# Performance work log

Measured on AMD Instinct MI355X. Metric: run time of the kernel, lower is better.

Reference implementation:

```python
import jax, jax.numpy as jnp
import numpy as np
from jax import lax

DN = ("NCDHW", "OIDHW", "NCDHW")


def bn(x, g, b, eps=1e-5):
    # torch BatchNorm3d training-mode forward: biased batch stats over (N, *, spatial)
    axes = (0,) + tuple(range(2, x.ndim))
    m = x.mean(axes, keepdims=True)
    v = x.var(axes, keepdims=True)
    shp = (1, -1) + (1,) * (x.ndim - 2)
    return (x - m) * lax.rsqrt(v + eps) * g.reshape(shp) + b.reshape(shp)


def conv_bn_relu(x, w, g, b, stride=(1, 1, 1), pad=(1, 0, 0)):
    y = lax.conv_general_dilated(x, w, stride, [(p, p) for p in pad], dimension_numbers=DN)
    return jax.nn.relu(bn(y, g, b))


def pw_bn_relu(x, w, g, b):  # 1x1x1 conv (no bias) + BN + ReLU on (B,C,T,H,W)
    y = jnp.einsum('oi,bithw->bothw', w, x)
    return jax.nn.relu(bn(y, g, b))


def pam_enc(x, pe_w, pe_g, pe_b):
    b, c, t, h, w = x.shape
    xm = x.mean(axis=2)  # all adaptive pools have T_out = 1
    feats = []
    for i, s in enumerate((1, 2, 3, 6)):  # H,W chosen divisible by 1,2,3,6 -> exact block means
        p = xm.reshape(b, c, s, h // s, s, w // s).mean(axis=(3, 5))  # (B,C,s,s)
        f = jnp.einsum('oi,bihw->bohw', pe_w[i], p)
        f = jax.nn.relu(bn(f, pe_g[i], pe_b[i]))
        feats.append(f.reshape(b, c, s * s))
    return jnp.concatenate(feats, axis=2)  # (B, C, 1+4+9+36=50)


def pam_dec(x, y, wq, bq, wk, bk, wv, bv, scale):
    # x: (B,C,T,H,W), y: (B,K,C)
    b, c, t, h, w = x.shape
    n = t * h * w
    q = jnp.einsum('oi,bithw->bothw', wq, x) + bq.reshape(1, -1, 1, 1, 1)
    q = q.reshape(b, c // 4, n).transpose(0, 2, 1)            # (B,N,C/4)
    k = y @ wk.T + bk                                         # (B,K,C/4)
    attn = jax.nn.softmax(jnp.einsum('bnd,bkd->bnk', q, k), axis=-1)
    v = y @ wv.T + bv                                         # (B,K,C)
    out = jnp.einsum('bkc,bnk->bcn', v, attn).reshape(b, c, t, h, w)
    return scale * out + x


def cam_dec(x, y, scale):
    b, c, t, h, w = x.shape
    xf = x.reshape(b, c, -1)
    yf = y.reshape(b, y.shape[1], -1)
    energy = jnp.einsum('bcn,bkn->bck', xf, yf)               # (B,C,K)
    attn = jax.nn.softmax(energy.max(-1, keepdims=True) - energy, axis=-1)
    out = jnp.einsum('bck,bkn->bcn', attn, yf).reshape(b, c, t, h, w)
    return x + scale * out


def tam_dec(x, y, scale):
    xp = x.transpose(0, 2, 1, 3, 4)  # (B,T,C,H,W)
    yp = y.transpose(0, 2, 1, 3, 4)
    b, t, c, h, w = xp.shape
    xf = xp.reshape(b, t, -1)
    yf = yp.reshape(b, t, -1)
    energy = jnp.einsum('bim,bjm->bij', xf, yf)               # (B,T,T)
    attn = jax.nn.softmax(energy.max(-1, keepdims=True) - energy, axis=-1)
    out = jnp.einsum('bij,bjm->bim', attn, yf).reshape(b, t, c, h, w)
    return (xp + scale * out).transpose(0, 2, 1, 3, 4)


def caf(x1, x2, w_conv1, g_conv1, b_conv1, w_conv2, g_conv2, b_conv2, w_tam, g_tam, b_tam, w_cat, g_cat, b_cat, pe_w, pe_g, pe_b, pd_wq, pd_bq, pd_wk, pd_bk, pd_wv, pd_bv, pd_scale, ce_w, ce_g, ce_b, cd_scale, te_w, te_g, te_b, td_scale):
    c1 = lambda z: conv_bn_relu(z, w_conv1, g_conv1, b_conv1)
    c2 = lambda z: conv_bn_relu(z, w_conv2, g_conv2, b_conv2)
    x1i = c1(x1)  # conv1(x1) is used by both PAM and CAM branches (identical in torch)
    x2i = c1(x2)
    # PAM branches
    x1_pa = c2(pam_dec(x1i, pam_enc(x1i, pe_w, pe_g, pe_b).transpose(0, 2, 1), pd_wq, pd_bq, pd_wk, pd_bk, pd_wv, pd_bv, pd_scale))
    x2_pa = c2(pam_dec(x2i, pam_enc(x2i, pe_w, pe_g, pe_b).transpose(0, 2, 1), pd_wq, pd_bq, pd_wk, pd_bk, pd_wv, pd_bv, pd_scale))
    # CAM branches
    x1_ca = c2(cam_dec(x1i, pw_bn_relu(x1i, ce_w, ce_g, ce_b), cd_scale))
    x2_ca = c2(cam_dec(x2i, pw_bn_relu(x2i, ce_w, ce_g, ce_b), cd_scale))
    # TAM branch over temporal concat (2T frames)
    xt1 = c1(jnp.concatenate([x1, x2], axis=2))
    xt2 = pw_bn_relu(xt1, te_w, te_g, te_b)
    x_ta = conv_bn_relu(tam_dec(xt1, xt2, td_scale), w_tam, g_tam, b_tam, stride=(2, 1, 1))
    out1 = conv_bn_relu(jnp.concatenate([x1_pa, x2_ca, x_ta], axis=1), w_cat, g_cat, b_cat)
    out2 = conv_bn_relu(jnp.concatenate([x2_pa, x1_ca, x_ta], axis=1), w_cat, g_cat, b_cat)
    return out1, out2


def setup_inputs() -> dict:
    key = jax.random.key(0)
    B, C, T, H, W = 4, 256, 16, 36, 36
    IC = C // 4
    ks = iter(jax.random.split(key, 24))
    rn = lambda shape, s=0.05: jax.random.normal(next(ks), shape, jnp.float32) * s
    ones = lambda n: jnp.ones((n,), jnp.float32)
    zeros = lambda n: jnp.zeros((n,), jnp.float32)
    return {
        "x1": rn((B, C, T, H, W), 1.0),
        "x2": rn((B, C, T, H, W), 1.0),
        "w_conv1": rn((IC, C, 3, 1, 1)), "g_conv1": ones(IC), "b_conv1": zeros(IC),
        "w_conv2": rn((IC, IC, 3, 1, 1)), "g_conv2": ones(IC), "b_conv2": zeros(IC),
        "w_tam": rn((IC, IC, 3, 1, 1)), "g_tam": ones(IC), "b_tam": zeros(IC),
        "w_cat": rn((C, 3 * IC, 3, 1, 1)), "g_cat": ones(C), "b_cat": zeros(C),
        "pe_w": rn((4, IC, IC)), "pe_g": jnp.ones((4, IC), jnp.float32), "pe_b": jnp.zeros((4, IC), jnp.float32),
        "pd_wq": rn((IC // 4, IC)), "pd_bq": zeros(IC // 4),
        "pd_wk": rn((IC // 4, IC)), "pd_bk": zeros(IC // 4),
        "pd_wv": rn((IC, IC)), "pd_bv": zeros(IC),
        "pd_scale": jnp.full((1,), 0.1, jnp.float32),
        "ce_w": rn((IC // 16, IC)), "ce_g": ones(IC // 16), "ce_b": zeros(IC // 16),
        "cd_scale": jnp.full((1,), 0.1, jnp.float32),
        "te_w": rn((IC, IC)), "te_g": ones(IC), "te_b": zeros(IC),
        "td_scale": jnp.full((1,), 0.1, jnp.float32),
    }


def reference(x1, x2, w_conv1, g_conv1, b_conv1, w_conv2, g_conv2, b_conv2, w_tam, g_tam, b_tam, w_cat, g_cat, b_cat, pe_w, pe_g, pe_b, pd_wq, pd_bq, pd_wk, pd_bk, pd_wv, pd_bv, pd_scale, ce_w, ce_g, ce_b, cd_scale, te_w, te_g, te_b, td_scale):
    return caf(x1, x2, w_conv1, g_conv1, b_conv1, w_conv2, g_conv2, b_conv2, w_tam, g_tam, b_tam, w_cat, g_cat, b_cat, pe_w, pe_g, pe_b, pd_wq, pd_bq, pd_wk, pd_bk, pd_wv, pd_bv, pd_scale, ce_w, ce_g, ce_b, cd_scale, te_w, te_g, te_b, td_scale)
```

## Files before the change

### kernel.cpp

```cpp
#include <hip/hip_runtime.h>

#define HW 1296
#define Tt 16
#define T2 32
#define Nn 20736
#define N2 41472
#define TAPAD 72

typedef short bf16x8 __attribute__((ext_vector_type(8)));
typedef float f32x4 __attribute__((ext_vector_type(4)));

__device__ inline unsigned short f2b(float f){
  union { float f; unsigned u; } v; v.f = f;
  unsigned r = v.u + 0x7FFF + ((v.u >> 16) & 1);
  return (unsigned short)(r >> 16);
}
__device__ inline float b2f(unsigned short u){
  union { unsigned u; float f; } v; v.u = ((unsigned)u) << 16; return v.f;
}
__device__ inline float b2f_lo(unsigned u){
  union { unsigned u; float f; } v; v.u = u << 16; return v.f;
}
__device__ inline float b2f_hi(unsigned u){
  union { unsigned u; float f; } v; v.u = u & 0xffff0000u; return v.f;
}

__device__ __forceinline__ void pack_pairs(const float* a, unsigned* vals){
  #pragma unroll
  for (int i = 0; i < 32; ++i)
    vals[i] = (unsigned)f2b(a[2*i]) | ((unsigned)f2b(a[2*i+1]) << 16);
}

__device__ __forceinline__ void staged_write(unsigned* lds, int tid, const unsigned* vals,
                                             uint4* o4, size_t R0, int rowu4, int cw,
                                             uint4* o4b){
  #pragma unroll
  for (int i = 0; i < 32; ++i) lds[tid*33 + i] = vals[i];
// ... 44 lines not shown
  if (idx < 12288){ wpack_one(idx, wt, Wpt, 64, 64, 3); return; }
  idx -= 12288;
  if (idx < 147456){ wpack_one(idx, wc, Wpc, 256, 192, 3); return; }
  idx -= 147456;
  if (idx < 4096){ wpack_one(idx, wte, Wpte, 64, 64, 1); return; }
  idx -= 4096;
  if (idx < 256){
    int o = idx / 64, i = idx % 64;
    wTce[i*4 + o] = wce[idx];
  }
}

__global__ void k_convT(const float* __restrict__ x1, const float* __restrict__ x2,
                        unsigned short* __restrict__ Pb){
  __shared__ unsigned lds[8448];
  int tid = threadIdx.x, z = blockIdx.z;
  int b = z & 3;
  const float* x = (z < 4) ? x1 : x2;
  int p0 = (z < 4) ? 0 : 16;
  int n0 = blockIdx.x*256, n = n0 + tid;
  const float* xb = x + (size_t)b*256*Nn + n;
  size_t R0 = (size_t)(b*32 + p0)*1296 + n0;
  uint4* o4 = (uint4*)Pb;
  for (int c0 = 0; c0 < 256; c0 += 64){
    float a[64];
    #pragma unroll
    for (int c = 0; c < 64; ++c) a[c] = xb[(size_t)(c0 + c)*Nn];
    unsigned vals[32];
    pack_pairs(a, vals);
    staged_write(lds, tid, vals, o4, R0, 32, c0 >> 3, nullptr);
  }
}

__launch_bounds__(256)
__global__ void k_mfconv(const unsigned short* __restrict__ P, const unsigned short* __restrict__ Wp,
                         float* __restrict__ out, int Cin, int Cout, int Mz,
                         int Tout, int stride, int KT, int pad, int p0, int plo, int phi, int PT,
                         float* __restrict__ sums, int obf)
{
  __shared__ float sred[2][4][4][16];
  int bz = blockIdx.z; int b = bz / Mz; int mz = bz - b*Mz;
  int lane = threadIdx.x & 63;
  int wave = threadIdx.x >> 6;
  int tile = blockIdx.x*4 + wave;
  bool valid = (tile < 27);
  int t = blockIdx.y;
  int col = lane & 15, grp = lane >> 4;
  int Kt32 = (KT*Cin) >> 5;
  f32x4 acc[4][3];
  #pragma unroll
  for (int i = 0; i < 4; ++i)
    #pragma unroll
    for (int j = 0; j < 3; ++j) acc[i][j] = (f32x4){0.f, 0.f, 0.f, 0.f};
  if (valid){
    int hw0 = tile*48 + col;
    const unsigned short* wbase = Wp + ((size_t)(mz*4)*Kt32)*512 + lane*8;
    for (int dt = 0; dt < KT; ++dt){
      int p = t*stride + dt - pad + p0;
      if (p < plo || p >= phi) continue;
      const unsigned short* Pp = P + ((size_t)(b*PT + p)*1296 + hw0)*Cin + grp*8;
      int nCk = Cin >> 5;
      int ksg = (dt*Cin) >> 5;
      for (int kc = 0; kc < nCk; ++kc){
        bf16x8 bf0 = *(const bf16x8*)(Pp + (size_t)0*Cin  + kc*32);
        bf16x8 bf1 = *(const bf16x8*)(Pp + (size_t)16*Cin + kc*32);
        bf16x8 bf2 = *(const bf16x8*)(Pp + (size_t)32*Cin + kc*32);
        #pragma unroll
        for (int mf = 0; mf < 4; ++mf){
          bf16x8 af = *(const bf16x8*)(wbase + ((size_t)mf*Kt32 + ksg + kc)*512);
          acc[mf][0] = __builtin_amdgcn_mfma_f32_16x16x32_bf16(af, bf0, acc[mf][0], 0, 0, 0);
          acc[mf][1] = __builtin_amdgcn_mfma_f32_16x16x32_bf16(af, bf1, acc[mf][1], 0, 0, 0);
          acc[mf][2] = __builtin_amdgcn_mfma_f32_16x16x32_bf16(af, bf2, acc[mf][2], 0, 0, 0);
        }
      }
    }
    size_t cs = (size_t)Tout*1296;
    size_t obase = ((size_t)(b*Cout + mz*64 + grp*4))*cs + (size_t)t*1296;
    if (obf){
      unsigned short* o16 = (unsigned short*)out;
      #pragma unroll
      for (int mf = 0; mf < 4; ++mf)
        #pragma unroll
        for (int f = 0; f < 3; ++f){
          int hw = tile*48 + f*16 + col;
          #pragma unroll
          for (int r = 0; r < 4; ++r)
            o16[obase + (size_t)(mf*16 + r)*cs + hw] = f2b(acc[mf][f][r]);
        }
    } else {
      #pragma unroll
      for (int mf = 0; mf < 4; ++mf)
        #pragma unroll
        for (int f = 0; f < 3; ++f){
          int hw = tile*48 + f*16 + col;
          #pragma unroll
          for (int r = 0; r < 4; ++r)
            out[obase + (size_t)(mf*16 + r)*cs + hw] = acc[mf][f][r];
        }
    }
  }
  float s[16], q[16];
  #pragma unroll
  for (int mf = 0; mf < 4; ++mf)
    #pragma unroll
    for (int r = 0; r < 4; ++r){
      float v0 = acc[mf][0][r], v1 = acc[mf][1][r], v2 = acc[mf][2][r];
      s[mf*4+r] = v0 + v1 + v2;
      q[mf*4+r] = v0*v0 + v1*v1 + v2*v2;
    }
  #pragma unroll
  for (int m = 1; m <= 8; m <<= 1){
    #pragma unroll
    for (int j = 0; j < 16; ++j){
      s[j] += __shfl_xor(s[j], m);
      q[j] += __shfl_xor(q[j], m);
    }
  }
  if (col == 0){
    #pragma unroll
    for (int j = 0; j < 16; ++j){
      sred[0][wave][grp][j] = s[j];
      sred[1][wave][grp][j] = q[j];
    }
  }
  __syncthreads();
  int tid = threadIdx.x;
  if (tid < 128){
    int stat = tid >> 6, ch = tid & 63;
    int rr = ch & 3, gg = (ch >> 2) & 3, mm = ch >> 4;
    int j = mm*4 + rr;
    float v = sred[stat][0][gg][j] + sred[stat][1][gg][j]
            + sred[stat][2][gg][j] + sred[stat][3][gg][j];
    atomicAdd(&sums[stat*Cout + mz*64 + ch], v);
  }
}

__global__ void k_tconv(const float* __restrict__ xA,
                        const float* __restrict__ wT,
                        float* __restrict__ out,
                        float* __restrict__ sums)
{
  __shared__ float r1[4][64], r2[4][64];
  int b  = blockIdx.z;
  int o  = threadIdx.x;
  int ty = threadIdx.y;
  int t  = blockIdx.y;
  int hw4 = blockIdx.x*64 + ty;
  bool valid = (hw4 < 324);
  float4 acc = make_float4(0.f,0.f,0.f,0.f);
  if (valid){
    const float4* xr = (const float4*)xA + ((size_t)b*64*16 + t)*324 + hw4;
    const float* wp  = wT + o;
    size_t xstep = (size_t)16*324;
    for (int i = 0; i < 64; ++i){
      float4 xv = *xr;
      float  wv = *wp;
      acc.x = fmaf(wv, xv.x, acc.x);
      acc.y = fmaf(wv, xv.y, acc.y);
      acc.z = fmaf(wv, xv.z, acc.z);
      acc.w = fmaf(wv, xv.w, acc.w);
      xr += xstep; wp += 4;
    }
    float4* op = (float4*)out + ((size_t)(b*4 + o)*16 + t)*324 + hw4;
    *op = acc;
  }
  r1[o][ty] = acc.x + acc.y + acc.z + acc.w;
  r2[o][ty] = acc.x*acc.x + acc.y*acc.y + acc.z*acc.z + acc.w*acc.w;
  __syncthreads();
  int tid = threadIdx.y*4 + threadIdx.x;
  for (int k = 32; k > 0; k >>= 1){
    if (ty < k){
      r1[o][ty] += r1[o][ty+k];
      r2[o][ty] += r2[o][ty+k];
    }
    __syncthreads();
  }
// ... 34 lines not shown
                             const unsigned short* __restrict__ x2bf,
                             const float* __restrict__ stats19,
                             const float* __restrict__ g,
                             const float* __restrict__ bet, float invc,
                             float* __restrict__ out)
{
  int z = blockIdx.z;
  int b = z & 3, which = z >> 2;
  const unsigned short* xbf = which ? x2bf : x1bf;
  const float* sums = stats19 + (size_t)which*512;
  float* op = out + (size_t)which*4*256*Nn;
  int c = blockIdx.y;
  int n8 = blockIdx.x*256 + threadIdx.x;
  if (n8 >= 2592) return;
  float m  = sums[c]*invc;
  float v  = fmaxf(sums[256+c]*invc - m*m, 0.f);
  float sc = g[c]*rsqrtf(v + 1e-5f);
  float bb = bet[c] - m*sc;
  size_t base = ((size_t)(b*256 + c))*Nn + (size_t)n8*8;
  uint4 u = *(const uint4*)(xbf + base);
  float4 o0, o1;
  o0.x = fmaxf(fmaf(b2f_lo(u.x), sc, bb), 0.f);
  o0.y = fmaxf(fmaf(b2f_hi(u.x), sc, bb), 0.f);
  o0.z = fmaxf(fmaf(b2f_lo(u.y), sc, bb), 0.f);
  o0.w = fmaxf(fmaf(b2f_hi(u.y), sc, bb), 0.f);
  o1.x = fmaxf(fmaf(b2f_lo(u.z), sc, bb), 0.f);
  o1.y = fmaxf(fmaf(b2f_hi(u.z), sc, bb), 0.f);
  o1.z = fmaxf(fmaf(b2f_lo(u.w), sc, bb), 0.f);
  o1.w = fmaxf(fmaf(b2f_hi(u.w), sc, bb), 0.f);
  *(float4*)(op + base) = o0;
  *(float4*)(op + base + 4) = o1;
}

__global__ void k_bnrelu_mean(float* __restrict__ x, const float* __restrict__ sums,
                              const float* __restrict__ g, const float* __restrict__ bet,
                              float invc, float* __restrict__ p6)
{
  __shared__ float p6loc[36];
  int tid = threadIdx.x;
  if (tid < 36) p6loc[tid] = 0.f;
  __syncthreads();
  int hw = blockIdx.x*256 + tid;
  int c = blockIdx.y, b = blockIdx.z;
  if (hw < 1296){
    float m  = sums[c]*invc;
    float v  = fmaxf(sums[64+c]*invc - m*m, 0.f);
    float sc = g[c]*rsqrtf(v + 1e-5f);
    float bb = bet[c] - m*sc;
    float* xb = x + ((size_t)(b*64 + c)*16)*1296 + hw;
    float s = 0.f;
    #pragma unroll
    for (int t = 0; t < 16; ++t){
      float val = fmaxf(fmaf(xb[(size_t)t*1296], sc, bb), 0.f);
      xb[(size_t)t*1296] = val;
      s += val;
    }
    int h = hw / 36, w = hw - h*36;
    atomicAdd(&p6loc[(h/6)*6 + (w/6)], s*(1.f/16.f));
  }
  __syncthreads();
  if (tid < 36) atomicAdd(&p6[((size_t)(b*64 + c))*36 + tid], p6loc[tid]);
}

__global__ void k_bnT(const void* __restrict__ xraw, const float* __restrict__ sums,
                      const float* __restrict__ g, const float* __restrict__ bet, float invc,
                      unsigned short* __restrict__ P1, unsigned short* __restrict__ P2,
                      int L, int outC, int coff, int xbf)
{
  __shared__ unsigned lds[8448];
  int tid = threadIdx.x, b = blockIdx.z;
  int n0 = blockIdx.x*256, n = n0 + tid;
  float a[64];
  if (xbf){
    const unsigned short* xb = (const unsigned short*)xraw + (size_t)b*64*L + n;
    #pragma unroll
    for (int c = 0; c < 64; ++c){
      float m  = sums[c]*invc;
      float vv = fmaxf(sums[64+c]*invc - m*m, 0.f);
      float sc = g[c]*rsqrtf(vv + 1e-5f);
      float bb = bet[c] - m*sc;
      a[c] = fmaxf(fmaf(b2f(xb[(size_t)c*L]), sc, bb), 0.f);
    }
  } else {
    const float* xb = (const float*)xraw + (size_t)b*64*L + n;
    #pragma unroll
    for (int c = 0; c < 64; ++c){
      float m  = sums[c]*invc;
      float vv = fmaxf(sums[64+c]*invc - m*m, 0.f);
      float sc = g[c]*rsqrtf(vv + 1e-5f);
      float bb = bet[c] - m*sc;
      a[c] = fmaxf(fmaf(xb[(size_t)c*L], sc, bb), 0.f);
    }
  }
  unsigned vals[32];
  pack_pairs(a, vals);
  staged_write(lds, tid, vals, (uint4*)P1, (size_t)b*L + n0, outC >> 3, coff >> 3,
               P2 ? (uint4*)P2 : nullptr);
}

__global__ void k_bnT_cc(const float* __restrict__ A, const float* __restrict__ M,
                         const float* __restrict__ B, const float* __restrict__ sums,
                         const float* __restrict__ g, const float* __restrict__ bet,
                         float invc, unsigned short* __restrict__ P1)
{
  __shared__ unsigned lds[8448];
  int tid = threadIdx.x, b = blockIdx.z;
  int n0 = blockIdx.x*256, n = n0 + tid;
  int t = n / 1296, hw = n - t*1296;
  const float* src; size_t cstride;
  if (t < 15){ src = A + ((size_t)(b*64)*16 + t)*1296 + hw; cstride = (size_t)16*1296; }
  else if (t < 17){ src = M + ((size_t)(b*64)*2 + (t-15))*1296 + hw; cstride = (size_t)2*1296; }
  else { src = B + ((size_t)(b*64)*16 + (t-16))*1296 + hw; cstride = (size_t)16*1296; }
  float a[64];
  #pragma unroll
  for (int c = 0; c < 64; ++c){
    float m  = sums[c]*invc;
    float vv = fmaxf(sums[64+c]*invc - m*m, 0.f);
    float sc = g[c]*rsqrtf(vv + 1e-5f);
    float bb = bet[c] - m*sc;
    a[c] = fmaxf(fmaf(src[c*cstride], sc, bb), 0.f);
  }
  unsigned vals[32];
  pack_pairs(a, vals);
  staged_write(lds, tid, vals, (uint4*)P1, (size_t)b*N2 + n0, 8, 0, nullptr);
}


__global__ void k_pamenc1(const float* __restrict__ p6, const float* __restrict__ pe_w,
                          float* __restrict__ pf, float* __restrict__ sl){
  __shared__ float psh[64];
  int cell = blockIdx.x, b = blockIdx.z;
  int o = threadIdx.x;
  int s, off;
  if (cell < 1){ s=1; off=0; } else if (cell < 5){ s=2; off=1; }
  else if (cell < 14){ s=3; off=5; } else { s=6; off=14; }
  int local = cell - off, ph = local/s, pw = local%s;
  int bs = 6/s;
  const float* pp = p6 + ((size_t)(b*64 + o))*36;
  float sum = 0.f;
  for (int i = 0; i < bs; ++i)
    for (int j = 0; j < bs; ++j)
      sum += pp[(ph*bs + i)*6 + (pw*bs + j)];
  psh[o] = sum * ((float)(s*s) * (1.f/1296.f));
  __syncthreads();
  int grp = (cell < 1) ? 0 : (cell < 5) ? 1 : (cell < 14) ? 2 : 3;
  const float* w = pe_w + (size_t)grp*4096 + o*64;
  float acc = 0.f;
  #pragma unroll
  for (int i = 0; i < 64; ++i) acc = fmaf(w[i], psh[i], acc);
  pf[((size_t)b*64 + o)*50 + cell] = acc;
  atomicAdd(&sl[grp*128 + o], acc);
  atomicAdd(&sl[grp*128 + 64 + o], acc*acc);
}

__launch_bounds__(128)
__global__ void k_pamenc2(const float* __restrict__ pf, const float* __restrict__ sl,
                          const float* __restrict__ pe_g, const float* __restrict__ pe_b,
                          const float* __restrict__ wk, const float* __restrict__ bk,
                          const float* __restrict__ wv, const float* __restrict__ bv,
                          const float* __restrict__ wq, const float* __restrict__ bq,
                          float* __restrict__ vb, float* __restrict__ KW,
                          float* __restrict__ sb)
{
  __shared__ float yk[64];
  __shared__ float kbl[16];
  int k = blockIdx.x, b = blockIdx.z;
  int tid = threadIdx.x;
  int grp = (k < 1) ? 0 : (k < 5) ? 1 : (k < 14) ? 2 : 3;
  const float ss2[4] = {1.f, 4.f, 9.f, 36.f};
  if (tid < 64){
    float invc = 1.f/(4.f*ss2[grp]);
    float m = sl[grp*128 + tid]*invc;
    float var = fmaxf(sl[grp*128 + 64 + tid]*invc - m*m, 0.f);
    float sc = pe_g[grp*64 + tid]*rsqrtf(var + 1e-5f);
    float sh = pe_b[grp*64 + tid] - m*sc;
    yk[tid] = fmaxf(fmaf(pf[((size_t)b*64 + tid)*50 + k], sc, sh), 0.f);
  }
  __syncthreads();
  if (tid < 16){
    float s = bk[tid];
    #pragma unroll
    for (int c = 0; c < 64; ++c) s = fmaf(wk[tid*64 + c], yk[c], s);
    kbl[tid] = s;
  } else if (tid < 80){
    int c = tid - 16;
    float s = bv[c];
    #pragma unroll
    for (int i = 0; i < 64; ++i) s = fmaf(wv[c*64 + i], yk[i], s);
    vb[((size_t)b*50 + k)*64 + c] = s;
  }
  __syncthreads();
  if (tid < 64){
    float s = 0.f;
    #pragma unroll
    for (int o = 0; o < 16; ++o) s = fmaf(kbl[o], wq[o*64 + tid], s);
    KW[((size_t)b*50 + k)*64 + tid] = s;
  } else if (tid == 64){
    float s = 0.f;
    #pragma unroll
    for (int o = 0; o < 16; ++o) s = fmaf(kbl[o], bq[o], s);
    sb[(size_t)b*50 + k] = s;
  }
}

__launch_bounds__(256, 1)
__global__ void k_pamattn(const float* __restrict__ x, const float* __restrict__ KW,
                          const float* __restrict__ sbb, const float* __restrict__ vbuf,
                          const float* __restrict__ scp, unsigned short* __restrict__ Pg)
{
  __shared__ unsigned smem_u[8448];
  float* smem = (float*)smem_u;
  int b = blockIdx.z, tid = threadIdx.x;
  for (int i = tid; i < 3200; i += 256){
    smem[i]        = KW[(size_t)b*3200 + i];
    smem[3200 + i] = vbuf[(size_t)b*3200 + i];
  }
  if (tid < 50) smem[6400 + tid] = sbb[(size_t)b*50 + tid];
  __syncthreads();
  int n0 = blockIdx.x*256;
  int n = n0 + tid;
  const float* xb = x + (size_t)b*64*Nn + n;
  float xv[64];
  #pragma unroll
  for (int c = 0; c < 64; ++c) xv[c] = xb[(size_t)c*Nn];
  float s[50];
  const float4* kw4 = (const float4*)smem;
  #pragma unroll
  for (int k = 0; k < 50; ++k){
    float t = smem[6400 + k];
    #pragma unroll
    for (int c4 = 0; c4 < 16; ++c4){
      float4 kw = kw4[k*16 + c4];
      t = fmaf(xv[c4*4+0], kw.x, t);
      t = fmaf(xv[c4*4+1], kw.y, t);
      t = fmaf(xv[c4*4+2], kw.z, t);
      t = fmaf(xv[c4*4+3], kw.w, t);
    }
    s[k] = t;
  }
  float mx = -1e30f;
  #pragma unroll
  for (int k = 0; k < 50; ++k) mx = fmaxf(mx, s[k]);
  float sum = 0.f;
  #pragma unroll
  for (int k = 0; k < 50; ++k){ float p = __expf(s[k]-mx); s[k] = p; sum += p; }
  float sc = scp[0]/sum;
  const float4* vl4 = (const float4*)(smem + 3200);
  #pragma unroll
  for (int k = 0; k < 50; ++k){
    float pk = sc * s[k];
    #pragma unroll
    for (int c4 = 0; c4 < 16; ++c4){
      float4 v = vl4[k*16 + c4];
      xv[c4*4+0] = fmaf(pk, v.x, xv[c4*4+0]);
      xv[c4*4+1] = fmaf(pk, v.y, xv[c4*4+1]);
      xv[c4*4+2] = fmaf(pk, v.z, xv[c4*4+2]);
      xv[c4*4+3] = fmaf(pk, v.w, xv[c4*4+3]);
    }
  }
  __syncthreads();
  unsigned vals[32];
  pack_pairs(xv, vals);
  staged_write(smem_u, tid, vals, (uint4*)Pg, (size_t)b*Nn + n0, 8, 0, nullptr);
}


__global__ void k_camenergy2(const float* __restrict__ x, const float* __restrict__ yc,
                             const float* __restrict__ sums, const float* __restrict__ ce_g,
                             const float* __restrict__ ce_b, float invc,
                             float* __restrict__ e){
  __shared__ float yl[4][256];
  int b = blockIdx.z, tid = threadIdx.x;
  int n0 = blockIdx.x*256;
  #pragma unroll
  for (int k = 0; k < 4; ++k){
    float m  = sums[k]*invc;
    float vv = fmaxf(sums[4+k]*invc - m*m, 0.f);
    float sck = ce_g[k]*rsqrtf(vv + 1e-5f);
    float bbk = ce_b[k] - m*sck;
    float raw = yc[((size_t)b*4+k)*Nn + n0 + tid];
    yl[k][tid] = fmaxf(fmaf(raw, sck, bbk), 0.f);
  }
  __syncthreads();
  int c = tid & 63, ks = tid >> 6;
  const float* xr = x + (size_t)(b*64+c)*Nn + n0;
  const float* yr = yl[ks];
  float acc = 0.f;
  #pragma unroll 8
  for (int i = 0; i < 256; ++i) acc = fmaf(xr[i], yr[i], acc);
  atomicAdd(&e[((size_t)(b*64)+c)*4 + ks], acc);
}

__global__ void k_camapplyT(const float* __restrict__ x, const float* __restrict__ yc,
                            const float* __restrict__ sums, const float* __restrict__ ce_g,
                            const float* __restrict__ ce_b, float invc,
                            const float* __restrict__ e, const float* __restrict__ scp,
                            unsigned short* __restrict__ Pg){
  __shared__ float pw[64][4];
  __shared__ unsigned lds[8448];
  int tid = threadIdx.x;
  int b = blockIdx.z;
  if (tid < 64){
    const float* er = e + (size_t)(b*64+tid)*4;
    float e0=er[0], e1=er[1], e2=er[2], e3=er[3];
    float mx = fmaxf(fmaxf(e0,e1), fmaxf(e2,e3));
    float z0=mx-e0, z1=mx-e1, z2=mx-e2, z3=mx-e3;
    float zm = fmaxf(fmaxf(z0,z1), fmaxf(z2,z3));
    float p0=__expf(z0-zm), p1=__expf(z1-zm), p2=__expf(z2-zm), p3=__expf(z3-zm);
    float inv = 1.f/(p0+p1+p2+p3);
    pw[tid][0]=p0*inv; pw[tid][1]=p1*inv; pw[tid][2]=p2*inv; pw[tid][3]=p3*inv;
  }
  __syncthreads();
  int n0 = blockIdx.x*256;
  int n = n0 + tid;
  float yv[4];
  #pragma unroll
  for (int k = 0; k < 4; ++k){
    float m  = sums[k]*invc;
    float vv = fmaxf(sums[4+k]*invc - m*m, 0.f);
    float sck = ce_g[k]*rsqrtf(vv + 1e-5f);
    float bbk = ce_b[k] - m*sck;
    yv[k] = fmaxf(fmaf(yc[((size_t)b*4+k)*Nn + n], sck, bbk), 0.f);
  }
  float sc = scp[0];
  const float* xb = x + (size_t)b*64*Nn + n;
  float a[64];
  #pragma unroll
  for (int c = 0; c < 64; ++c){
    a[c] = fmaf(sc, pw[c][0]*yv[0] + pw[c][1]*yv[1] + pw[c][2]*yv[2] + pw[c][3]*yv[3],
                xb[(size_t)c*Nn]);
  }
  unsigned vals[32];
  pack_pairs(a, vals);
  staged_write(lds, tid, vals, (uint4*)Pg, (size_t)b*Nn + n0, 8, 0, nullptr);
}


__launch_bounds__(256)
__global__ void k_tamenergy_mf(const unsigned short* __restrict__ X,
                               const unsigned short* __restrict__ Y,
                               float* __restrict__ E){
  int b = blockIdx.z;
  int wave = threadIdx.x >> 6, lane = threadIdx.x & 63;
  int r = lane & 15, g = lane >> 4;
  const unsigned short* Xb = X + (size_t)b*32*82944;
  const unsigned short* Yb = Y + (size_t)b*32*82944;
  f32x4 a00 = (f32x4){0.f,0.f,0.f,0.f};
  f32x4 a01 = a00, a10 = a00, a11 = a00;
  int c0 = (blockIdx.x*4 + wave)*8;
  for (int cc = 0; cc < 8; ++cc){
    size_t k0 = (size_t)(c0 + cc)*32 + (size_t)g*8;
    bf16x8 x0 = *(const bf16x8*)(Xb + (size_t)r*82944 + k0);
    bf16x8 x1 = *(const bf16x8*)(Xb + (size_t)(r+16)*82944 + k0);
    bf16x8 y0 = *(const bf16x8*)(Yb + (size_t)r*82944 + k0);
    bf16x8 y1 = *(const bf16x8*)(Yb + (size_t)(r+16)*82944 + k0);
    a00 = __builtin_amdgcn_mfma_f32_16x16x32_bf16(x0, y0, a00, 0, 0, 0);
    a01 = __builtin_amdgcn_mfma_f32_16x16x32_bf16(x0, y1, a01, 0, 0, 0);
    a10 = __builtin_amdgcn_mfma_f32_16x16x32_bf16(x1, y0, a10, 0, 0, 0);
    a11 = __builtin_amdgcn_mfma_f32_16x16x32_bf16(x1, y1, a11, 0, 0, 0);
  }
  float* Eb = E + (size_t)b*1024;
  #pragma unroll
  for (int rr = 0; rr < 4; ++rr){
    int row = g*4 + rr;
    atomicAdd(&Eb[row*32 + r],           a00[rr]);
    atomicAdd(&Eb[row*32 + 16 + r],      a01[rr]);
    atomicAdd(&Eb[(row+16)*32 + r],      a10[rr]);
// ... 95 lines not shown
  const float* pe_w    = (const float*)d_in[14];
  const float* pe_g    = (const float*)d_in[15];
  const float* pe_b    = (const float*)d_in[16];
  const float* pd_wq   = (const float*)d_in[17];
  const float* pd_bq   = (const float*)d_in[18];
  const float* pd_wk   = (const float*)d_in[19];
  const float* pd_bk   = (const float*)d_in[20];
  const float* pd_wv   = (const float*)d_in[21];
  const float* pd_bv   = (const float*)d_in[22];
  const float* pd_scale= (const float*)d_in[23];
  const float* ce_w    = (const float*)d_in[24];
  const float* ce_g    = (const float*)d_in[25];
  const float* ce_b    = (const float*)d_in[26];
  const float* cd_scale= (const float*)d_in[27];
  const float* te_w    = (const float*)d_in[28];
  const float* te_g    = (const float*)d_in[29];
  const float* te_b    = (const float*)d_in[30];
  const float* td_scale= (const float*)d_in[31];

  float* ws = (float*)d_ws;
  size_t off = 0;
  auto alloc = [&](size_t n){ float* p = ws + off; off += (n + 3) & ~(size_t)3; return p; };
  float* stats = alloc(16384);
  float* e_tam = alloc(4096);
  float* e_cam = alloc(2048);
  float* p6a   = alloc(9216);
  float* p6b   = alloc(9216);
  float* wTce  = alloc(256);
  unsigned short* Wp1  = (unsigned short*)alloc(24576);
  unsigned short* Wp2  = (unsigned short*)alloc(6144);
  unsigned short* Wpt  = (unsigned short*)alloc(6144);
  unsigned short* Wpc  = (unsigned short*)alloc(73728);
  unsigned short* Wpte = (unsigned short*)alloc(2048);
  float* pfb   = alloc(12800);
  float* vb    = alloc(12800);
  float* KWb   = alloc(12800);
  float* sbb   = alloc(256);
  float* yc    = alloc(331776);
  float* Mb    = alloc(663552);
  float* A     = alloc(5308416);
  float* Bb    = alloc(5308416);
  float* PTEf  = alloc(5308416);
  float* COMB  = alloc(31850496);

  unsigned short* P0 = (unsigned short*)COMB;
  unsigned short* DdBF = (unsigned short*)COMB;
  unsigned short* Dbf  = (unsigned short*)(COMB + 10616832);
  unsigned short* PTAM = (unsigned short*)(COMB + 15925248);
  unsigned short* RrawBF = (unsigned short*)COMB;
  unsigned short* PCAT1 = (unsigned short*)(COMB + 5308416);
  unsigned short* PCAT2 = (unsigned short*)(COMB + 13271040);
  unsigned short* PG    = (unsigned short*)(COMB + 21233664);
  unsigned short* CATR1 = (unsigned short*)(COMB + 21233664);
  unsigned short* CATR2 = (unsigned short*)A;
  unsigned short* PTE = (unsigned short*)PTEf;

  const float invc16 = 1.f/(4.f*20736.f);
  const float invc32 = 1.f/(4.f*41472.f);

  k_zero<<<dim3(160), 256, 0, stream>>>(stats, 40960);
  k_wprep<<<dim3(881), 256, 0, stream>>>(w_conv1, w_conv2, w_tam, w_cat, te_w, ce_w,
                                         Wp1, Wp2, Wpt, Wpc, Wpte, wTce);
  k_convT<<<dim3(81, 1, 8), 256, 0, stream>>>(x1, x2, P0);

  k_mfconv<<<dim3(7,16,4), 256, 0, stream>>>(P0, Wp1, A,  256, 64, 1, 16, 1, 3, 1, 0, 0, 16, 32, stats + 0*512, 0);
  k_mfconv<<<dim3(7,16,4), 256, 0, stream>>>(P0, Wp1, Bb, 256, 64, 1, 16, 1, 3, 1, 16, 16, 32, 32, stats + 1*512, 0);
  k_mfconv<<<dim3(7,2,4),  256, 0, stream>>>(P0, Wp1, Mb, 256, 64, 1, 2, 1, 3, 1, 15, 0, 32, 32, stats + 21*512, 0);
  k_planestats<<<dim3(1,64,2), 256, 0, stream>>>(A, Bb, stats + 22*512, stats + 23*512);
  k_combine<<<dim3(1), 128, 0, stream>>>(stats);
  k_bnT_cc<<<dim3(162,1,4), 256, 0, stream>>>(A, Mb, Bb, stats + 2*512,
                                              g_conv1, b_conv1, invc32, PTE);

  k_mfconv<<<dim3(7,32,4), 256, 0, stream>>>(PTE, Wpte, (float*)DdBF, 64, 64, 1, 32, 1, 1, 0, 0, 0, 32, 32, stats + 3*512, 1);
  k_bnT<<<dim3(162,1,4), 256, 0, stream>>>(DdBF, stats + 3*512, te_g, te_b, invc32,
                                           Dbf, nullptr, N2, 64, 0, 1);

  k_tamenergy_mf<<<dim3(81, 1, 4), 256, 0, stream>>>(PTE, Dbf, e_tam);
  k_tamapply_mf<<<dim3(162, 1, 4), 256, 0, stream>>>(PTE, Dbf, e_tam, td_scale, PTAM);
  k_mfconv<<<dim3(7,16,4), 256, 0, stream>>>(PTAM, Wpt, (float*)RrawBF, 64, 64, 1, 16, 2, 3, 1, 0, 0, 32, 32, stats + 4*512, 1);
  k_bnT<<<dim3(81,1,4), 256, 0, stream>>>(RrawBF, stats + 4*512, g_tam, b_tam, invc16,
                                          PCAT1, PCAT2, Nn, 192, 128, 1);

  auto pam = [&](float* xin, const float* p6, unsigned short* catp, int slot_pe, int slot_c2){
    k_pamenc1<<<dim3(50, 1, 4), 64, 0, stream>>>(p6, pe_w, pfb, stats + (size_t)slot_pe*512);
    k_pamenc2<<<dim3(50, 1, 4), 128, 0, stream>>>(pfb, stats + (size_t)slot_pe*512,
                                                  pe_g, pe_b, pd_wk, pd_bk, pd_wv, pd_bv,
                                                  pd_wq, pd_bq, vb, KWb, sbb);
    k_pamattn<<<dim3(81, 1, 4), 256, 0, stream>>>(xin, KWb, sbb, vb, pd_scale, PG);
    k_mfconv<<<dim3(7,16,4), 256, 0, stream>>>(PG, Wp2, (float*)RrawBF, 64, 64, 1, 16, 1, 3, 1, 0, 0, 16, 16, stats + (size_t)slot_c2*512, 1);
    k_bnT<<<dim3(81,1,4), 256, 0, stream>>>(RrawBF, stats + (size_t)slot_c2*512,
                                            g_conv2, b_conv2, invc16, catp, nullptr, Nn, 192, 0, 1);
  };
  auto cam = [&](const float* xin, unsigned short* catp, float* ecam,
                 int slot_ce, int slot_c2){
    float* sums_ce = stats + (size_t)slot_ce*512;
    k_tconv<<<dim3(6, 16, 4), dim3(4, 64), 0, stream>>>(xin, wTce, yc, sums_ce);
    k_camenergy2<<<dim3(81, 1, 4), 256, 0, stream>>>(xin, yc, sums_ce, ce_g, ce_b, invc16, ecam);
    k_camapplyT<<<dim3(81, 1, 4), 256, 0, stream>>>(xin, yc, sums_ce, ce_g, ce_b, invc16,
                                                    ecam, cd_scale, PG);
    k_mfconv<<<dim3(7,16,4), 256, 0, stream>>>(PG, Wp2, (float*)RrawBF, 64, 64, 1, 16, 1, 3, 1, 0, 0, 16, 16, stats + (size_t)slot_c2*512, 1);
    k_bnT<<<dim3(81,1,4), 256, 0, stream>>>(RrawBF, stats + (size_t)slot_c2*512,
                                            g_conv2, b_conv2, invc16, catp, nullptr, Nn, 192, 64, 1);
  };

  k_bnrelu_mean<<<dim3(6,64,4), 256, 0, stream>>>(A, stats + 0*512, g_conv1, b_conv1,
                                                  invc16, p6a);
  pam(A, p6a, PCAT1, 5, 13);
  cam(A, PCAT2, e_cam, 15, 17);
  k_bnrelu_mean<<<dim3(6,64,4), 256, 0, stream>>>(Bb, stats + 1*512, g_conv1, b_conv1,
                                                  invc16, p6b);
  pam(Bb, p6b, PCAT2, 9, 14);
  cam(Bb, PCAT1, e_cam + 1024, 16, 18);

  k_mfconv<<<dim3(7,16,16), 256, 0, stream>>>(PCAT1, Wpc, (float*)CATR1, 192, 256, 4, 16, 1, 3, 1, 0, 0, 16, 16, stats + 19*512, 1);
  k_mfconv<<<dim3(7,16,16), 256, 0, stream>>>(PCAT2, Wpc, (float*)CATR2, 192, 256, 4, 16, 1, 3, 1, 0, 0, 16, 16, stats + 20*512, 1);
  k_bnrelu_out<<<dim3(11, 256, 8), 256, 0, stream>>>(CATR1, CATR2, stats + 19*512,
                                                     g_cat, b_cat, invc16, (float*)d_out);
}
```

Before: 925.9 us.

## Batch branch-wise kernel launches into merged grids over both inputs and stages

Several kernels that were launched separately for the A and B branches (and for PAM/CAM stages) now run once over a doubled or quadrupled blockIdx.z. This covers conv1, BN-mean, the PAM encoders and attention, CAM tconv, energy and apply, conv2 and BN, and the concat conv. The goal is to cut launch count and to fill the GPU better, since each launch previously had only a few hundred blocks. In exchange it needs more scratch buffers (doubled pf/vb/KW/yc and a 4-stage PG4) and reuses the A buffer as R4, which adds aliasing risk.

```diff
diff --git a/kernel.cpp b/kernel.cpp
--- a/kernel.cpp
+++ b/kernel.cpp
@@ -1,8 +1,6 @@
 #include <hip/hip_runtime.h>
 
 #define HW 1296
-#define Tt 16
-#define T2 32
 #define Nn 20736
 #define N2 41472
 #define TAPAD 72
@@ -113,14 +111,14 @@
   }
 }
 
-__launch_bounds__(256)
-__global__ void k_mfconv(const unsigned short* __restrict__ P, const unsigned short* __restrict__ Wp,
-                         float* __restrict__ out, int Cin, int Cout, int Mz,
-                         int Tout, int stride, int KT, int pad, int p0, int plo, int phi, int PT,
-                         float* __restrict__ sums, int obf)
-{
-  __shared__ float sred[2][4][4][16];
-  int bz = blockIdx.z; int b = bz / Mz; int mz = bz - b*Mz;
+__device__ __forceinline__ void mf_body(const unsigned short* __restrict__ P,
+                                        const unsigned short* __restrict__ Wp,
+                                        void* __restrict__ out, float* __restrict__ sums,
+                                        float* sredf,
+                                        int Cin, int Cout, int mz, int b,
+                                        int Tout, int stride, int KT, int pad,
+                                        int p0, int plo, int phi, int PT, int obf)
+{
   int lane = threadIdx.x & 63;
   int wave = threadIdx.x >> 6;
   int tile = blockIdx.x*4 + wave;
@@ -169,6 +167,7 @@
             o16[obase + (size_t)(mf*16 + r)*cs + hw] = f2b(acc[mf][f][r]);
         }
     } else {
+      float* o32 = (float*)out;
       #pragma unroll
       for (int mf = 0; mf < 4; ++mf)
         #pragma unroll
@@ -176,7 +175,7 @@
           int hw = tile*48 + f*16 + col;
           #pragma unroll
           for (int r = 0; r < 4; ++r)
-            out[obase + (size_t)(mf*16 + r)*cs + hw] = acc[mf][f][r];
+            o32[obase + (size_t)(mf*16 + r)*cs + hw] = acc[mf][f][r];
         }
     }
   }
@@ -200,8 +199,8 @@
   if (col == 0){
     #pragma unroll
     for (int j = 0; j < 16; ++j){
-      sred[0][wave][grp][j] = s[j];
-      sred[1][wave][grp][j] = q[j];
+      sredf[((0*4 + wave)*4 + grp)*16 + j] = s[j];
+      sredf[((1*4 + wave)*4 + grp)*16 + j] = q[j];
     }
   }
   __syncthreads();
@@ -210,19 +209,75 @@
     int stat = tid >> 6, ch = tid & 63;
     int rr = ch & 3, gg = (ch >> 2) & 3, mm = ch >> 4;
     int j = mm*4 + rr;
-    float v = sred[stat][0][gg][j] + sred[stat][1][gg][j]
-            + sred[stat][2][gg][j] + sred[stat][3][gg][j];
+    float v = sredf[((stat*4 + 0)*4 + gg)*16 + j] + sredf[((stat*4 + 1)*4 + gg)*16 + j]
+            + sredf[((stat*4 + 2)*4 + gg)*16 + j] + sredf[((stat*4 + 3)*4 + gg)*16 + j];
     atomicAdd(&sums[stat*Cout + mz*64 + ch], v);
   }
 }
 
-__global__ void k_tconv(const float* __restrict__ xA,
-                        const float* __restrict__ wT,
-                        float* __restrict__ out,
-                        float* __restrict__ sums)
+__launch_bounds__(256)
+__global__ void k_mfconv(const unsigned short* __restrict__ P, const unsigned short* __restrict__ Wp,
+                         float* __restrict__ out, int Cin, int Cout, int Mz,
+                         int Tout, int stride, int KT, int pad, int p0, int plo, int phi, int PT,
+                         float* __restrict__ sums, int obf)
+{
+  __shared__ float sred[2*4*4*16];
+  int bz = blockIdx.z; int b = bz / Mz; int mz = bz - b*Mz;
+  mf_body(P, Wp, out, sums, sred, Cin, Cout, mz, b, Tout, stride, KT, pad,
+          p0, plo, phi, PT, obf);
+}
+
+__launch_bounds__(256)
+__global__ void k_mfconv_ab(const unsigned short* __restrict__ P, const unsigned short* __restrict__ Wp,
+                            float* __restrict__ A, float* __restrict__ Bb,
+                            float* __restrict__ stats)
+{
+  __shared__ float sred[2*4*4*16];
+  int bz = blockIdx.z; int which = bz >> 2; int b = bz & 3;
+  float* out = which ? Bb : A;
+  float* sums = stats + (size_t)which*512;
+  int p0 = which*16;
+  mf_body(P, Wp, out, sums, sred, 256, 64, 0, b, 16, 1, 3, 1, p0, p0, p0+16, 32, 0);
+}
+
+__launch_bounds__(256)
+__global__ void k_mfconv4(const unsigned short* __restrict__ PG4, const unsigned short* __restrict__ Wp,
+                          unsigned short* __restrict__ Rout, float* __restrict__ stats)
+{
+  __shared__ float sred[2*4*4*16];
+  int pb = blockIdx.z;
+  int stage = pb >> 2;
+  int slot = (stage < 2) ? (13 + stage) : (15 + stage);
+  mf_body(PG4, Wp, Rout, stats + (size_t)slot*512, sred, 64, 64, 0, pb,
+          16, 1, 3, 1, 0, 0, 16, 16, 1);
+}
+
+__launch_bounds__(256)
+__global__ void k_mfconvcat(const unsigned short* __restrict__ PCAT1, const unsigned short* __restrict__ PCAT2,
+                            const unsigned short* __restrict__ Wp,
+                            unsigned short* __restrict__ CATR1, unsigned short* __restrict__ CATR2,
+                            float* __restrict__ stats)
+{
+  __shared__ float sred[2*4*4*16];
+  int bz = blockIdx.z;
+  int which = bz >> 4; int rem = bz & 15;
+  int b = rem >> 2; int mz = rem & 3;
+  const unsigned short* P = which ? PCAT2 : PCAT1;
+  unsigned short* out = which ? CATR2 : CATR1;
+  float* sums = stats + (size_t)(19 + which)*512;
+  mf_body(P, Wp, out, sums, sred, 192, 256, mz, b, 16, 1, 3, 1, 0, 0, 16, 16, 1);
+}
+
+__global__ void k_tconvm(const float* __restrict__ A, const float* __restrict__ Bb,
+                         const float* __restrict__ wT,
+                         float* __restrict__ yc2, float* __restrict__ stats)
 {
   __shared__ float r1[4][64], r2[4][64];
-  int b  = blockIdx.z;
+  int z = blockIdx.z;
+  int which = z >> 2, b = z & 3;
+  const float* xA = which ? Bb : A;
+  float* out = yc2 + (size_t)which*331776;
+  float* sums = stats + (size_t)(15 + which)*512;
   int o  = threadIdx.x;
   int ty = threadIdx.y;
   int t  = blockIdx.y;
@@ -323,16 +378,22 @@
   *(float4*)(op + base + 4) = o1;
 }
 
-__global__ void k_bnrelu_mean(float* __restrict__ x, const float* __restrict__ sums,
-                              const float* __restrict__ g, const float* __restrict__ bet,
-                              float invc, float* __restrict__ p6)
+__global__ void k_bnrelu_mean2(float* __restrict__ A, float* __restrict__ Bb,
+                               const float* __restrict__ stats,
+                               const float* __restrict__ g, const float* __restrict__ bet,
+                               float invc, float* __restrict__ p6a, float* __restrict__ p6b)
 {
   __shared__ float p6loc[36];
+  int z = blockIdx.z;
+  int which = z >> 2, b = z & 3;
+  float* x = which ? Bb : A;
+  const float* sums = stats + (size_t)which*512;
+  float* p6 = which ? p6b : p6a;
   int tid = threadIdx.x;
   if (tid < 36) p6loc[tid] = 0.f;
   __syncthreads();
   int hw = blockIdx.x*256 + tid;
-  int c = blockIdx.y, b = blockIdx.z;
+  int c = blockIdx.y;
   if (hw < 1296){
     float m  = sums[c]*invc;
     float v  = fmaxf(sums[64+c]*invc - m*m, 0.f);
@@ -387,6 +448,34 @@
   pack_pairs(a, vals);
   staged_write(lds, tid, vals, (uint4*)P1, (size_t)b*L + n0, outC >> 3, coff >> 3,
                P2 ? (uint4*)P2 : nullptr);
+}
+
+__global__ void k_bnT4(const unsigned short* __restrict__ R4, const float* __restrict__ stats,
+                       const float* __restrict__ g, const float* __restrict__ bet, float invc,
+                       unsigned short* __restrict__ PCAT1, unsigned short* __restrict__ PCAT2)
+{
+  __shared__ unsigned lds[8448];
+  int z = blockIdx.z;
+  int stage = z >> 2, b = z & 3;
+  int slot = (stage < 2) ? (13 + stage) : (15 + stage);
+  const float* sums = stats + (size_t)slot*512;
+  unsigned short* P1 = (stage == 0 || stage == 3) ? PCAT1 : PCAT2;
+  int cw = (stage < 2) ? 0 : 8;
+  int tid = threadIdx.x;
+  int n0 = blockIdx.x*256, n = n0 + tid;
+  const unsigned short* xb = R4 + (size_t)z*64*Nn + n;
+  float a[64];
+  #pragma unroll
+  for (int c = 0; c < 64; ++c){
+    float m  = sums[c]*invc;
+    float vv = fmaxf(sums[64+c]*invc - m*m, 0.f);
+    float sc = g[c]*rsqrtf(vv + 1e-5f);
+    float bb = bet[c] - m*sc;
+    a[c] = fmaxf(fmaf(b2f(xb[(size_t)c*Nn]), sc, bb), 0.f);
+  }
+  unsigned vals[32];
+  pack_pairs(a, vals);
+  staged_write(lds, tid, vals, (uint4*)P1, (size_t)b*Nn + n0, 24, cw, nullptr);
 }
 
 __global__ void k_bnT_cc(const float* __restrict__ A, const float* __restrict__ M,
@@ -417,10 +506,16 @@
 }
 
 
-__global__ void k_pamenc1(const float* __restrict__ p6, const float* __restrict__ pe_w,
-                          float* __restrict__ pf, float* __restrict__ sl){
+__global__ void k_pamenc1m(const float* __restrict__ p6a, const float* __restrict__ p6b,
+                           const float* __restrict__ pe_w,
+                           float* __restrict__ pf2, float* __restrict__ stats){
   __shared__ float psh[64];
-  int cell = blockIdx.x, b = blockIdx.z;
+  int z = blockIdx.z;
+  int which = z >> 2, b = z & 3;
+  const float* p6 = which ? p6b : p6a;
+  float* sl = stats + (size_t)(which ? 9 : 5)*512;
+  float* pf = pf2 + (size_t)which*12800;
+  int cell = blockIdx.x;
   int o = threadIdx.x;
   int s, off;
   if (cell < 1){ s=1; off=0; } else if (cell < 5){ s=2; off=1; }
@@ -445,17 +540,24 @@
 }
 
 __launch_bounds__(128)
-__global__ void k_pamenc2(const float* __restrict__ pf, const float* __restrict__ sl,
-                          const float* __restrict__ pe_g, const float* __restrict__ pe_b,
-                          const float* __restrict__ wk, const float* __restrict__ bk,
-                          const float* __restrict__ wv, const float* __restrict__ bv,
-                          const float* __restrict__ wq, const float* __restrict__ bq,
-                          float* __restrict__ vb, float* __restrict__ KW,
-                          float* __restrict__ sb)
+__global__ void k_pamenc2m(const float* __restrict__ pf2, float* __restrict__ stats,
+                           const float* __restrict__ pe_g, const float* __restrict__ pe_b,
+                           const float* __restrict__ wk, const float* __restrict__ bk,
+                           const float* __restrict__ wv, const float* __restrict__ bv,
+                           const float* __restrict__ wq, const float* __restrict__ bq,
+                           float* __restrict__ vb2, float* __restrict__ KW2,
+                           float* __restrict__ sb2)
 {
   __shared__ float yk[64];
   __shared__ float kbl[16];
-  int k = blockIdx.x, b = blockIdx.z;
+  int z = blockIdx.z;
+  int which = z >> 2, b = z & 3;
+  const float* pf = pf2 + (size_t)which*12800;
+  const float* sl = stats + (size_t)(which ? 9 : 5)*512;
+  float* vb = vb2 + (size_t)which*12800;
+  float* KW = KW2 + (size_t)which*12800;
+  float* sb = sb2 + (size_t)which*256;
+  int k = blockIdx.x;
   int tid = threadIdx.x;
   int grp = (k < 1) ? 0 : (k < 5) ? 1 : (k < 14) ? 2 : 3;
   const float ss2[4] = {1.f, 4.f, 9.f, 36.f};
@@ -495,13 +597,20 @@
 }
 
 __launch_bounds__(256, 1)
-__global__ void k_pamattn(const float* __restrict__ x, const float* __restrict__ KW,
-                          const float* __restrict__ sbb, const float* __restrict__ vbuf,
-                          const float* __restrict__ scp, unsigned short* __restrict__ Pg)
+__global__ void k_pamattnm(const float* __restrict__ A, const float* __restrict__ Bb,
+                           const float* __restrict__ KW2, const float* __restrict__ sb2,
+                           const float* __restrict__ vb2, const float* __restrict__ scp,
+                           unsigned short* __restrict__ PG4)
 {
   __shared__ unsigned smem_u[8448];
   float* smem = (float*)smem_u;
-  int b = blockIdx.z, tid = threadIdx.x;
+  int z = blockIdx.z;
+  int which = z >> 2, b = z & 3;
+  const float* x = which ? Bb : A;
+  const float* KW = KW2 + (size_t)which*12800;
+  const float* sbb = sb2 + (size_t)which*256;
+  const float* vbuf = vb2 + (size_t)which*12800;
+  int tid = threadIdx.x;
   for (int i = tid; i < 3200; i += 256){
     smem[i]        = KW[(size_t)b*3200 + i];
     smem[3200 + i] = vbuf[(size_t)b*3200 + i];
@@ -552,16 +661,22 @@
   __syncthreads();
   unsigned vals[32];
   pack_pairs(xv, vals);
-  staged_write(smem_u, tid, vals, (uint4*)Pg, (size_t)b*Nn + n0, 8, 0, nullptr);
-}
-
-
-__global__ void k_camenergy2(const float* __restrict__ x, const float* __restrict__ yc,
-                             const float* __restrict__ sums, const float* __restrict__ ce_g,
-                             const float* __restrict__ ce_b, float invc,
-                             float* __restrict__ e){
+  staged_write(smem_u, tid, vals, (uint4*)PG4, (size_t)(which*4 + b)*Nn + n0, 8, 0, nullptr);
+}
+
+
+__global__ void k_camenergy2m(const float* __restrict__ A, const float* __restrict__ Bb,
+                              const float* __restrict__ yc2, const float* __restrict__ stats,
+                              const float* __restrict__ ce_g, const float* __restrict__ ce_b,
+                              float invc, float* __restrict__ e_cam){
   __shared__ float yl[4][256];
-  int b = blockIdx.z, tid = threadIdx.x;
+  int z = blockIdx.z;
+  int which = z >> 2, b = z & 3;
+  const float* x = which ? Bb : A;
+  const float* yc = yc2 + (size_t)which*331776;
+  const float* sums = stats + (size_t)(15 + which)*512;
+  float* e = e_cam + (size_t)which*1024;
+  int tid = threadIdx.x;
   int n0 = blockIdx.x*256;
   #pragma unroll
   for (int k = 0; k < 4; ++k){
@@ -582,15 +697,20 @@
   atomicAdd(&e[((size_t)(b*64)+c)*4 + ks], acc);
 }
 
-__global__ void k_camapplyT(const float* __restrict__ x, const float* __restrict__ yc,
-                            const float* __restrict__ sums, const float* __restrict__ ce_g,
-                            const float* __restrict__ ce_b, float invc,
-                            const float* __restrict__ e, const float* __restrict__ scp,
-                            unsigned short* __restrict__ Pg){
+__global__ void k_camapplyTm(const float* __restrict__ A, const float* __restrict__ Bb,
+                             const float* __restrict__ yc2, const float* __restrict__ stats,
+                             const float* __restrict__ ce_g, const float* __restrict__ ce_b,
+                             float invc, const float* __restrict__ e_cam,
+                             const float* __restrict__ scp, unsigned short* __restrict__ PG4){
   __shared__ float pw[64][4];
   __shared__ unsigned lds[8448];
+  int z = blockIdx.z;
+  int which = z >> 2, b = z & 3;
+  const float* x = which ? Bb : A;
+  const float* yc = yc2 + (size_t)which*331776;
+  const float* sums = stats + (size_t)(15 + which)*512;
+  const float* e = e_cam + (size_t)which*1024;
   int tid = threadIdx.x;
-  int b = blockIdx.z;
   if (tid < 64){
     const float* er = e + (size_t)(b*64+tid)*4;
     float e0=er[0], e1=er[1], e2=er[2], e3=er[3];
@@ -623,7 +743,7 @@
   }
   unsigned vals[32];
   pack_pairs(a, vals);
-  staged_write(lds, tid, vals, (uint4*)Pg, (size_t)b*Nn + n0, 8, 0, nullptr);
+  staged_write(lds, tid, vals, (uint4*)PG4, (size_t)((2+which)*4 + b)*Nn + n0, 8, 0, nullptr);
 }
 
 
@@ -785,11 +905,11 @@
   unsigned short* Wpt  = (unsigned short*)alloc(6144);
   unsigned short* Wpc  = (unsigned short*)alloc(73728);
   unsigned short* Wpte = (unsigned short*)alloc(2048);
-  float* pfb   = alloc(12800);
-  float* vb    = alloc(12800);
-  float* KWb   = alloc(12800);
-  float* sbb   = alloc(256);
-  float* yc    = alloc(331776);
+  float* pf2   = alloc(25600);
+  float* vb2   = alloc(25600);
+  float* KW2   = alloc(25600);
+  float* sb2   = alloc(512);
+  float* yc2   = alloc(663552);
   float* Mb    = alloc(663552);
   float* A     = alloc(5308416);
   float* Bb    = alloc(5308416);
@@ -803,7 +923,8 @@
   unsigned short* RrawBF = (unsigned short*)COMB;
   unsigned short* PCAT1 = (unsigned short*)(COMB + 5308416);
   unsigned short* PCAT2 = (unsigned short*)(COMB + 13271040);
-  unsigned short* PG    = (unsigned short*)(COMB + 21233664);
+  unsigned short* PG4   = (unsigned short*)(COMB + 21233664);
+  unsigned short* R4    = (unsigned short*)A;
   unsigned short* CATR1 = (unsigned short*)(COMB + 21233664);
   unsigned short* CATR2 = (unsigned short*)A;
   unsigned short* PTE = (unsigned short*)PTEf;
@@ -816,9 +937,8 @@
                                          Wp1, Wp2, Wpt, Wpc, Wpte, wTce);
   k_convT<<<dim3(81, 1, 8), 256, 0, stream>>>(x1, x2, P0);
 
-  k_mfconv<<<dim3(7,16,4), 256, 0, stream>>>(P0, Wp1, A,  256, 64, 1, 16, 1, 3, 1, 0, 0, 16, 32, stats + 0*512, 0);
-  k_mfconv<<<dim3(7,16,4), 256, 0, stream>>>(P0, Wp1, Bb, 256, 64, 1, 16, 1, 3, 1, 16, 16, 32, 32, stats + 1*512, 0);
-  k_mfconv<<<dim3(7,2,4),  256, 0, stream>>>(P0, Wp1, Mb, 256, 64, 1, 2, 1, 3, 1, 15, 0, 32, 32, stats + 21*512, 0);
+  k_mfconv_ab<<<dim3(7,16,8), 256, 0, stream>>>(P0, Wp1, A, Bb, stats);
+  k_mfconv<<<dim3(7,2,4), 256, 0, stream>>>(P0, Wp1, Mb, 256, 64, 1, 2, 1, 3, 1, 15, 0, 32, 32, stats + 21*512, 0);
   k_planestats<<<dim3(1,64,2), 256, 0, stream>>>(A, Bb, stats + 22*512, stats + 23*512);
   k_combine<<<dim3(1), 128, 0, stream>>>(stats);
   k_bnT_cc<<<dim3(162,1,4), 256, 0, stream>>>(A, Mb, Bb, stats + 2*512,
@@ -834,39 +954,24 @@
   k_bnT<<<dim3(81,1,4), 256, 0, stream>>>(RrawBF, stats + 4*512, g_tam, b_tam, invc16,
                                           PCAT1, PCAT2, Nn, 192, 128, 1);
 
-  auto pam = [&](float* xin, const float* p6, unsigned short* catp, int slot_pe, int slot_c2){
-    k_pamenc1<<<dim3(50, 1, 4), 64, 0, stream>>>(p6, pe_w, pfb, stats + (size_t)slot_pe*512);
-    k_pamenc2<<<dim3(50, 1, 4), 128, 0, stream>>>(pfb, stats + (size_t)slot_pe*512,
-                                                  pe_g, pe_b, pd_wk, pd_bk, pd_wv, pd_bv,
-                                                  pd_wq, pd_bq, vb, KWb, sbb);
-    k_pamattn<<<dim3(81, 1, 4), 256, 0, stream>>>(xin, KWb, sbb, vb, pd_scale, PG);
-    k_mfconv<<<dim3(7,16,4), 256, 0, stream>>>(PG, Wp2, (float*)RrawBF, 64, 64, 1, 16, 1, 3, 1, 0, 0, 16, 16, stats + (size_t)slot_c2*512, 1);
-    k_bnT<<<dim3(81,1,4), 256, 0, stream>>>(RrawBF, stats + (size_t)slot_c2*512,
-                                            g_conv2, b_conv2, invc16, catp, nullptr, Nn, 192, 0, 1);
-  };
-  auto cam = [&](const float* xin, unsigned short* catp, float* ecam,
-                 int slot_ce, int slot_c2){
-    float* sums_ce = stats + (size_t)slot_ce*512;
-    k_tconv<<<dim3(6, 16, 4), dim3(4, 64), 0, stream>>>(xin, wTce, yc, sums_ce);
-    k_camenergy2<<<dim3(81, 1, 4), 256, 0, stream>>>(xin, yc, sums_ce, ce_g, ce_b, invc16, ecam);
-    k_camapplyT<<<dim3(81, 1, 4), 256, 0, stream>>>(xin, yc, sums_ce, ce_g, ce_b, invc16,
-                                                    ecam, cd_scale, PG);
-    k_mfconv<<<dim3(7,16,4), 256, 0, stream>>>(PG, Wp2, (float*)RrawBF, 64, 64, 1, 16, 1, 3, 1, 0, 0, 16, 16, stats + (size_t)slot_c2*512, 1);
-    k_bnT<<<dim3(81,1,4), 256, 0, stream>>>(RrawBF, stats + (size_t)slot_c2*512,
-                                            g_conv2, b_conv2, invc16, catp, nullptr, Nn, 192, 64, 1);
-  };
-
-  k_bnrelu_mean<<<dim3(6,64,4), 256, 0, stream>>>(A, stats + 0*512, g_conv1, b_conv1,
-                                                  invc16, p6a);
-  pam(A, p6a, PCAT1, 5, 13);
-  cam(A, PCAT2, e_cam, 15, 17);
-  k_bnrelu_mean<<<dim3(6,64,4), 256, 0, stream>>>(Bb, stats + 1*512, g_conv1, b_conv1,
-                                                  invc16, p6b);
-  pam(Bb, p6b, PCAT2, 9, 14);
-  cam(Bb, PCAT1, e_cam + 1024, 16, 18);
-
-  k_mfconv<<<dim3(7,16,16), 256, 0, stream>>>(PCAT1, Wpc, (float*)CATR1, 192, 256, 4, 16, 1, 3, 1, 0, 0, 16, 16, stats + 19*512, 1);
-  k_mfconv<<<dim3(7,16,16), 256, 0, stream>>>(PCAT2, Wpc, (float*)CATR2, 192, 256, 4, 16, 1, 3, 1, 0, 0, 16, 16, stats + 20*512, 1);
+  k_bnrelu_mean2<<<dim3(6,64,8), 256, 0, stream>>>(A, Bb, stats, g_conv1, b_conv1,
+                                                   invc16, p6a, p6b);
+  k_pamenc1m<<<dim3(50,1,8), 64, 0, stream>>>(p6a, p6b, pe_w, pf2, stats);
+  k_pamenc2m<<<dim3(50,1,8), 128, 0, stream>>>(pf2, stats, pe_g, pe_b,
+                                               pd_wk, pd_bk, pd_wv, pd_bv, pd_wq, pd_bq,
+                                               vb2, KW2, sb2);
+  k_pamattnm<<<dim3(81,1,8), 256, 0, stream>>>(A, Bb, KW2, sb2, vb2, pd_scale, PG4);
+  k_tconvm<<<dim3(6,16,8), dim3(4,64), 0, stream>>>(A, Bb, wTce, yc2, stats);
+  k_camenergy2m<<<dim3(81,1,8), 256, 0, stream>>>(A, Bb, yc2, stats, ce_g, ce_b,
+                                                  invc16, e_cam);
+  k_camapplyTm<<<dim3(81,1,8), 256, 0, stream>>>(A, Bb, yc2, stats, ce_g, ce_b,
+                                                 invc16, e_cam, cd_scale, PG4);
+
+  k_mfconv4<<<dim3(7,16,16), 256, 0, stream>>>(PG4, Wp2, R4, stats);
+  k_bnT4<<<dim3(81,1,16), 256, 0, stream>>>(R4, stats, g_conv2, b_conv2, invc16,
+                                            PCAT1, PCAT2);
+
+  k_mfconvcat<<<dim3(7,16,32), 256, 0, stream>>>(PCAT1, PCAT2, Wpc, CATR1, CATR2, stats);
   k_bnrelu_out<<<dim3(11, 256, 8), 256, 0, stream>>>(CATR1, CATR2, stats + 19*512,
                                                      g_cat, b_cat, invc16, (float*)d_out);
 }
```

Measured after the change: 742.5 us (median of 4 runs). 19.8% less time.
